# Kernel optimization log

Hardware: AMD Instinct MI355X
Metric: run time of the kernel (lower is better)

## Reference

```python
import jax, jax.numpy as jnp
import numpy as np

NUM_BINS = 8
TAIL = 3.0
MBW = 0.001  # min_bin_width
MBH = 0.001  # min_bin_height
MD = 0.001   # min_derivative


def _conv(x, w, b):
    y = jax.lax.conv_general_dilated(x, w, (1, 1), 'SAME',
                                     dimension_numbers=('NCHW', 'OIHW', 'NCHW'))
    return y + b[None, :, None, None]


def _convnet(x, w1, b1, w2, b2, w3, b3):
    h = jax.nn.relu(_conv(x, w1, b1))
    h = jax.nn.relu(_conv(h, w2, b2))
    return _conv(h, w3, b3)


def _rqs_forward(x, uw, uh, ud):
    # x: (N,), uw/uh: (N, num_bins), ud: (N, num_bins-1)
    nb = uw.shape[-1]
    inside = (x >= -TAIL) & (x <= TAIL)
    xin = jnp.clip(x, -TAIL, TAIL)
    # linear tails: pad derivatives so boundary slope == 1
    const = float(np.log(np.exp(1.0 - MD) - 1.0))
    ud = jnp.pad(ud, ((0, 0), (1, 1)), constant_values=const)

    widths = jax.nn.softmax(uw, axis=-1)
    widths = MBW + (1.0 - MBW * nb) * widths
    cumw = jnp.pad(jnp.cumsum(widths, axis=-1), ((0, 0), (1, 0)))
    cumw = 2.0 * TAIL * cumw - TAIL
    cumw = cumw.at[:, 0].set(-TAIL).at[:, -1].set(TAIL)
    widths = cumw[:, 1:] - cumw[:, :-1]

    heights = jax.nn.softmax(uh, axis=-1)
    heights = MBH + (1.0 - MBH * nb) * heights
    cumh = jnp.pad(jnp.cumsum(heights, axis=-1), ((0, 0), (1, 0)))
    cumh = 2.0 * TAIL * cumh - TAIL
    cumh = cumh.at[:, 0].set(-TAIL).at[:, -1].set(TAIL)
    heights = cumh[:, 1:] - cumh[:, :-1]

    deriv = MD + jax.nn.softplus(ud)  # (N, nb+1)

    # searchsorted: locate bin of each element
    idx = jnp.clip(jnp.sum((xin[:, None] >= cumw).astype(jnp.int32), axis=-1) - 1, 0, nb - 1)
    gather = lambda t: jnp.take_along_axis(t, idx[:, None], axis=-1)[:, 0]

    in_cw = gather(cumw)
    in_w = gather(widths)
    in_ch = gather(cumh)
    in_h = gather(heights)
    in_delta = gather(heights / widths)
    d0 = gather(deriv)
    d1 = gather(deriv[:, 1:])

    theta = (xin - in_cw) / in_w
    tom = theta * (1.0 - theta)
    numer = in_h * (in_delta * theta ** 2 + d0 * tom)
    denom = in_delta + (d0 + d1 - 2.0 * in_delta) * tom
    y = in_ch + numer / denom
    dnum = in_delta ** 2 * (d1 * theta ** 2 + 2.0 * in_delta * tom + d0 * (1.0 - theta) ** 2)
    lad = jnp.log(dnum) - 2.0 * jnp.log(denom)

    y = jnp.where(inside, y, x)
    lad = jnp.where(inside, lad, 0.0)
    return y, lad


def setup_inputs() -> dict:
    key = jax.random.key(0)
    ks = jax.random.split(key, 9)
    B, C, H, W = 32, 12, 64, 64
    hidden = 128
    cond_c = C // 3
    out_spline = C * (3 * NUM_BINS - 1)
    x = jax.random.normal(ks[0], (B, C, H, W), dtype=jnp.float32)
    logdet = jnp.zeros((B,), dtype=jnp.float32)
    conditioning = jax.random.normal(ks[1], (B, cond_c, H, W), dtype=jnp.float32)
    w1 = jax.random.normal(ks[2], (hidden, C + cond_c, 3, 3), dtype=jnp.float32) * 0.05
    b1 = jnp.zeros((hidden,), dtype=jnp.float32)
    w2 = jax.random.normal(ks[3], (hidden, hidden, 1, 1), dtype=jnp.float32) * 0.05
    b2 = jnp.zeros((hidden,), dtype=jnp.float32)
    w3 = jax.random.normal(ks[4], (out_spline, hidden, 3, 3), dtype=jnp.float32) * 0.01
    b3 = jnp.zeros((out_spline,), dtype=jnp.float32)
    return {"x": x, "logdet": logdet, "conditioning": conditioning,
            "w1": w1, "b1": b1, "w2": w2, "b2": b2, "w3": w3, "b3": b3}


def reference(x, logdet, conditioning, w1, b1, w2, b2, w3, b3):
    B, C, H, W = x.shape
    net_in = jnp.concatenate([x, conditioning], axis=1)
    params = _convnet(net_in, w1, b1, w2, b2, w3, b3)  # (B, C*(3nb-1), H, W)
    params = params.reshape(B, C, 3 * NUM_BINS - 1, H, W)
    params = params.transpose(0, 1, 3, 4, 2).reshape(B * C * H * W, 3 * NUM_BINS - 1)
    uw = params[:, :NUM_BINS]
    uh = params[:, NUM_BINS:2 * NUM_BINS]
    ud = params[:, 2 * NUM_BINS:]
    y_flat, lad_flat = _rqs_forward(x.reshape(-1), uw, uh, ud)
    y = y_flat.reshape(B, C, H, W)
    logdet_out = logdet + lad_flat.reshape(B, -1).sum(axis=1)
    return y, logdet_out
```

## Files before the change

### kernel.cpp

```cpp
#include <hip/hip_runtime.h>
#include <math.h>


#define NPIX 4096
#define NY   1572864

typedef _Float16 half8 __attribute__((ext_vector_type(8)));
typedef _Float16 half4 __attribute__((ext_vector_type(4)));
typedef float f32x4 __attribute__((ext_vector_type(4)));

#define ASYNC16(gsrc, ldst) \
  __builtin_amdgcn_global_load_lds((const __attribute__((address_space(1))) unsigned int*)(gsrc), \
                                   (__attribute__((address_space(3))) unsigned int*)(ldst), 16, 0, 0)

#define H2P_PLANE 4356
#define H2P_IDX(b, cc, pp) ((((size_t)(b) * 4 + (cc)) * H2P_PLANE + (pp)) << 5)
#define XH_IDX(b, pp) (((size_t)(b) * H2P_PLANE + (pp)) << 5)

__global__ __launch_bounds__(256) void prep_xh_k(
    const float* __restrict__ w1, const float* __restrict__ w2,
    const float* __restrict__ w3, _Float16* __restrict__ w1h,
    _Float16* __restrict__ w2h, _Float16* __restrict__ w3h,
    const float* __restrict__ logdet, float* __restrict__ ld_out,
    const float* __restrict__ x, const float* __restrict__ cond,
    _Float16* __restrict__ xh)
{
    const int i = blockIdx.x * 256 + threadIdx.x;
    if (i < 36864) {
        int k = i & 31, oc = (i >> 5) & 127, t = i >> 12;
        w1h[i] = (_Float16)((k < 16) ? w1[(oc * 16 + k) * 9 + t] : 0.f);
    }
    if (i < 16384) {
        int km = i & 31, oc = (i >> 5) & 127, ks = i >> 12;
        w2h[i] = (_Float16)w2[oc * 128 + ks * 32 + km];
    }
    {
        int cim = i & 31;
        int oc = (i >> 5) % 288;
        int tc = i / (288 * 32);
        int t = tc >> 2, cc = tc & 3;
        int c = oc / 24, j = oc % 24;
        int ci = cc * 32 + cim;
        float v = (j < 23) ? w3[((c * 23 + j) * 128 + ci) * 9 + t] : 0.f;
        w3h[i] = (_Float16)v;
    }
    if (i < 32) ld_out[i] = logdet[i];

    if (i < 139392) {
        const int b = i / H2P_PLANE, pp = i % H2P_PLANE;
        const int pr = pp / 66, pc = pp % 66;
        const bool interior = (pr >= 1) && (pr <= 64) && (pc >= 1) && (pc <= 64);
        _Float16 v[32];
#pragma unroll
        for (int ci = 0; ci < 32; ++ci) v[ci] = (_Float16)0.f;
        if (interior) {
            const int p = (pr - 1) * 64 + (pc - 1);
#pragma unroll
            for (int ci = 0; ci < 12; ++ci)
                v[ci] = (_Float16)x[((size_t)(b * 12 + ci) << 12) + p];
#pragma unroll
            for (int ci = 0; ci < 4; ++ci)
                v[12 + ci] = (_Float16)cond[((size_t)(b * 4 + ci) << 12) + p];
        }
        _Float16* dst = xh + ((size_t)i << 5);
#pragma unroll
        for (int q = 0; q < 4; ++q) *(f32x4*)(dst + q * 8) = *(f32x4*)(v + q * 8);
    }
}

__global__ __launch_bounds__(256, 2) void conv1_k(
    const _Float16* __restrict__ xh, const _Float16* __restrict__ w1h,
    const float* __restrict__ b1, _Float16* __restrict__ h1p)
{
    __shared__ __align__(16) char smem[73728];
    const int tid = threadIdx.x;
    const int wv = tid >> 6, lane = tid & 63;
    const int row16 = lane & 15, quad = lane >> 4;
    const int ptile = blockIdx.x;
    const int b = ptile >> 4;
    const int pim0 = (ptile & 15) << 8;
    const int h0 = pim0 >> 6;

#pragma unroll
    for (int k = 0; k < 18; ++k)
        ASYNC16(w1h + (size_t)(k * 256 + tid) * 8, smem + (k * 256 + wv * 64) * 16);

    f32x4 acc[4][8];
#pragma unroll
    for (int pt = 0; pt < 4; ++pt)
#pragma unroll
        for (int ot = 0; ot < 8; ++ot) acc[pt][ot] = (f32x4){0.f, 0.f, 0.f, 0.f};

    __syncthreads();
    const _Float16* wl = (const _Float16*)smem;

    for (int t = 0; t < 9; ++t) {
        const int dy = t / 3, dx = t % 3;
        const int pbase = (h0 + wv + dy) * 66 + dx + row16;
        half8 bf[4], af[8];
#pragma unroll
        for (int pt = 0; pt < 4; ++pt)
            bf[pt] = *(const half8*)(xh + XH_IDX(b, pbase + pt * 16) + quad * 8);
#pragma unroll
        for (int ot = 0; ot < 8; ++ot)
            af[ot] = *(const half8*)(wl + ((t * 128 + ot * 16 + row16) << 5) + quad * 8);
#pragma unroll
        for (int ot = 0; ot < 8; ++ot)
#pragma unroll
            for (int pt = 0; pt < 4; ++pt)
                acc[pt][ot] = __builtin_amdgcn_mfma_f32_16x16x32_f16(af[ot], bf[pt], acc[pt][ot], 0, 0, 0);
    }

    f32x4 bias[8];
#pragma unroll
    for (int ot = 0; ot < 8; ++ot) bias[ot] = *(const f32x4*)(b1 + ot * 16 + quad * 4);
#pragma unroll
    for (int pt = 0; pt < 4; ++pt) {
        const size_t pbase = ((size_t)((b << 12) + pim0 + wv * 64 + pt * 16 + row16)) << 7;
#pragma unroll
        for (int ot = 0; ot < 8; ++ot) {
            half4 v;
#pragma unroll
            for (int r = 0; r < 4; ++r)
                v[r] = (_Float16)fmaxf(acc[pt][ot][r] + bias[ot][r], 0.f);
            *(half4*)(h1p + pbase + ot * 16 + quad * 4) = v;
        }
    }
}

__global__ __launch_bounds__(256, 3) void conv2_k(
    const _Float16* __restrict__ h1p, const _Float16* __restrict__ w2h,
    const float* __restrict__ b2, _Float16* __restrict__ h2p)
{
    __shared__ __align__(16) char smem[33280];
    float* b2l = (float*)(smem + 32768);
    const int tid = threadIdx.x;
    const int wv = tid >> 6, lane = tid & 63;
    const int row16 = lane & 15, quad = lane >> 4;
    const int ptile = blockIdx.x;
    const int b = ptile >> 4;
    const int pim0 = (ptile & 15) << 8;

    if (tid < 128) b2l[tid] = b2[tid];
#pragma unroll
    for (int k = 0; k < 8; ++k) {
        const int c0 = k * 256 + wv * 64;
        ASYNC16(w2h + (size_t)(c0 + lane) * 8, smem + c0 * 16);
    }

    {
        const int base = blockIdx.x * 256 + tid;
#pragma unroll
        for (int rep = 0; rep < 2; ++rep) {
            const int i = base + rep * 131072;
            if (i < 133120) {
                const int q = i & 3;
                const int rest = i >> 2;
                const int r = rest % 260;
                const int cc2 = (rest / 260) & 3;
                const int bb = rest / 1040;
                int pp;
                if (r < 66)       pp = r;
                else if (r < 132) pp = 65 * 66 + (r - 66);
                else if (r < 196) pp = (r - 131) * 66;
                else              pp = (r - 195) * 66 + 65;
                f32x4 z = {0.f, 0.f, 0.f, 0.f};
                *(f32x4*)(h2p + H2P_IDX(bb, cc2, pp) + q * 8) = z;
            }
        }
    }

    f32x4 acc[4][8];
#pragma unroll
    for (int pt = 0; pt < 4; ++pt)
#pragma unroll
        for (int ot = 0; ot < 8; ++ot) acc[pt][ot] = (f32x4){0.f, 0.f, 0.f, 0.f};

    const int pixbase = (b << 12) + pim0 + wv * 64;
    __syncthreads();

#pragma unroll
    for (int ks = 0; ks < 4; ++ks) {
        half8 bf[4], af[8];
#pragma unroll
        for (int pt = 0; pt < 4; ++pt)
            bf[pt] = *(const half8*)(h1p + ((size_t)(pixbase + pt * 16 + row16) << 7) + ks * 32 + quad * 8);
        const _Float16* wl = (const _Float16*)smem;
#pragma unroll
        for (int ot = 0; ot < 8; ++ot)
            af[ot] = *(const half8*)(wl + ((ks * 128 + ot * 16 + row16) << 5) + quad * 8);
#pragma unroll
        for (int ot = 0; ot < 8; ++ot)
#pragma unroll
            for (int pt = 0; pt < 4; ++pt)
                acc[pt][ot] = __builtin_amdgcn_mfma_f32_16x16x32_f16(af[ot], bf[pt], acc[pt][ot], 0, 0, 0);
    }

#pragma unroll
    for (int pt = 0; pt < 4; ++pt) {
        const int p = pim0 + wv * 64 + pt * 16 + row16;
        const int pp = ((p >> 6) + 1) * 66 + (p & 63) + 1;
#pragma unroll
        for (int ot = 0; ot < 8; ++ot) {
            const int oc0 = ot * 16 + quad * 4;
            half4 v;
#pragma unroll
            for (int r = 0; r < 4; ++r)
                v[r] = (_Float16)fmaxf(acc[pt][ot][r] + b2l[oc0 + r], 0.f);
            *(half4*)(h2p + H2P_IDX(b, oc0 >> 5, pp) + (oc0 & 31)) = v;
        }
    }
}

__device__ __forceinline__ void rqs_eval(const f32x4* pv, float xv,
                                         float& yv_out, float& lad_out)
{
#define PRM(j) (pv[(j) >> 2][(j) & 3])
    const float xin = fminf(fmaxf(xv, -3.f), 3.f);

    float mw = PRM(0), mh = PRM(8);
#pragma unroll
    for (int j = 1; j < 8; ++j) { mw = fmaxf(mw, PRM(j)); mh = fmaxf(mh, PRM(8 + j)); }
    float ew[8], eh[8];
    float sw = 0.f, sh = 0.f;
#pragma unroll
    for (int j = 0; j < 8; ++j) {
        ew[j] = __expf(PRM(j) - mw);      sw += ew[j];
        eh[j] = __expf(PRM(8 + j) - mh);  sh += eh[j];
    }
    const float rw = 1.f / sw, rh = 1.f / sh;

    const float CONST_D = 0.5397423f;

    float cumw = 0.f, cumh = 0.f;
    float cw_lo = -3.f, ch_lo = -3.f;
    float in_cw = 0.f, in_w = 1.f, in_ch = 0.f, in_h = 1.f, sd0 = 0.f, sd1 = 0.f;
#pragma unroll
    for (int i = 0; i < 8; ++i) {
        cumw += fmaf(0.992f, ew[i] * rw, 0.001f);
        cumh += fmaf(0.992f, eh[i] * rh, 0.001f);
        const float cw_hi = (i == 7) ? 3.f : fmaf(6.f, cumw, -3.f);
        const float ch_hi = (i == 7) ? 3.f : fmaf(6.f, cumh, -3.f);
        const bool sel = (xin >= cw_lo) && ((i == 7) || (xin < cw_hi));
        in_cw = sel ? cw_lo : in_cw;
        in_w  = sel ? (cw_hi - cw_lo) : in_w;
        in_ch = sel ? ch_lo : in_ch;
        in_h  = sel ? (ch_hi - ch_lo) : in_h;
        sd0   = sel ? ((i == 0) ? CONST_D : PRM(16 + i - 1)) : sd0;
        sd1   = sel ? ((i == 7) ? CONST_D : PRM(16 + i)) : sd1;
        cw_lo = cw_hi; ch_lo = ch_hi;
    }

    const float d0 = 0.001f + ((sd0 > 20.f) ? sd0 : __logf(1.f + __expf(sd0)));
    const float d1 = 0.001f + ((sd1 > 20.f) ? sd1 : __logf(1.f + __expf(sd1)));

    const float r_inw = 1.f / in_w;
    const float delta = in_h * r_inw;
    const float theta = (xin - in_cw) * r_inw;
    const float omt = 1.f - theta;
    const float tom = theta * omt;
    const float th2 = theta * theta;
    const float numer = in_h * (delta * th2 + d0 * tom);
    const float denom = delta + (d0 + d1 - 2.f * delta) * tom;
    const float rden = 1.f / denom;
    float yv = in_ch + numer * rden;
    const float dnum = delta * delta * (d1 * th2 + 2.f * delta * tom + d0 * omt * omt);
    float lad = __logf(dnum * rden * rden);

    const bool inside = (xv >= -3.f) && (xv <= 3.f);
    yv_out = inside ? yv : xv;
    lad_out = inside ? lad : 0.f;
#undef PRM
}

__global__ __launch_bounds__(256, 2) void conv3_rqs_k(
    const _Float16* __restrict__ h2p, const _Float16* __restrict__ w3h,
    const float* __restrict__ b3, const float* __restrict__ x,
    float* __restrict__ y, float* __restrict__ ld_out)
{
    __shared__ __align__(16) char smem[62592];
    float* b3l = (float*)(smem + 62208);

    const int tid = threadIdx.x;
    const int wv = tid >> 6, lane = tid & 63;
    const int row16 = lane & 15, quad = lane >> 4;
    const int bid = blockIdx.x;
    const int g = bid / 24, r = bid % 24;
    const int col = r >> 3;
    const int ptile = (g << 3) | (r & 7);
    const int b = ptile >> 4;
    const int pim0 = (ptile & 15) << 8;
    const int h0 = pim0 >> 6;

    if (tid < 96) {
        const int c = tid / 24, j = tid % 24;
        b3l[tid] = (j < 23) ? b3[(col * 4 + c) * 23 + j] : 0.f;
    }

    f32x4 acc[4][6];
#pragma unroll
    for (int pt = 0; pt < 4; ++pt)
#pragma unroll
        for (int ot = 0; ot < 6; ++ot) acc[pt][ot] = (f32x4){0.f, 0.f, 0.f, 0.f};

    auto stage_wt3 = [&](int dy, int cc, int buf) {
#pragma unroll
        for (int j = 0; j < 3; ++j) {
            const int t = dy * 3 + j;
            const _Float16* gp = w3h + ((size_t)((t * 4 + cc) * 288 + col * 96) << 5);
            char* wb = smem + 25344 + buf * 18432 + j * 6144;
            ASYNC16(gp + (size_t)tid * 8, wb + wv * 1024);
            if (wv < 2) ASYNC16(gp + (size_t)(256 + tid) * 8, wb + 4096 + wv * 1024);
        }
    };
    auto stage_act = [&](int cc) {
        const _Float16* ga = h2p + H2P_IDX(b, cc, h0 * 66);
#pragma unroll
        for (int k = 0; k < 6; ++k)
            ASYNC16(ga + (size_t)(k * 256 + tid) * 8, smem + (k * 256 + wv * 64) * 16);
        if (wv == 0 && lane < 48)
            ASYNC16(ga + (size_t)(1536 + lane) * 8, smem + 1536 * 16);
    };

    stage_act(0);
    stage_wt3(0, 0, 0);

    for (int cc = 0; cc < 4; ++cc) {
        for (int dy = 0; dy < 3; ++dy) {
            const int step = cc * 3 + dy;
            __syncthreads();
            if (step + 1 < 12)
                stage_wt3((dy == 2) ? 0 : dy + 1, (dy == 2) ? cc + 1 : cc, (step + 1) & 1);
            const _Float16* act = (const _Float16*)smem;
            const _Float16* wt = (const _Float16*)(smem + 25344 + (step & 1) * 18432);
            const int lrow = (wv + dy) * 66 + row16;
#pragma unroll
            for (int dx = 0; dx < 3; ++dx) {
                half8 bf[4], af[6];
#pragma unroll
                for (int pt = 0; pt < 4; ++pt)
                    bf[pt] = *(const half8*)(act + ((lrow + dx + pt * 16) << 5) + quad * 8);
#pragma unroll
                for (int ot = 0; ot < 6; ++ot)
                    af[ot] = *(const half8*)(wt + dx * 3072 + ((ot * 16 + row16) << 5) + quad * 8);
#pragma unroll
                for (int ot = 0; ot < 6; ++ot)
#pragma unroll
                    for (int pt = 0; pt < 4; ++pt)
                        acc[pt][ot] = __builtin_amdgcn_mfma_f32_16x16x32_f16(af[ot], bf[pt], acc[pt][ot], 0, 0, 0);
            }
            if (dy == 2 && cc < 3) {
                __syncthreads();
                stage_act(cc + 1);
            }
        }
    }
    __syncthreads();

    float* epi = (float*)smem + wv * 1600;
    float lad_acc = 0.f;
#pragma unroll
    for (int pt = 0; pt < 4; ++pt) {
#pragma unroll
        for (int ot = 0; ot < 6; ++ot)
            *(f32x4*)(epi + row16 * 100 + ot * 16 + quad * 4) = acc[pt][ot];
        asm volatile("s_waitcnt lgkmcnt(0)" ::: "memory");
        __builtin_amdgcn_sched_barrier(0);
        {
            const int p16 = lane & 15, c = lane >> 4;
            const float* pb = epi + p16 * 100 + c * 24;
            const float* bb = b3l + c * 24;
            f32x4 pv[6];
#pragma unroll
            for (int q = 0; q < 6; ++q)
                pv[q] = *(const f32x4*)(pb + q * 4) + *(const f32x4*)(bb + q * 4);
            const int tpix = wv * 64 + pt * 16 + p16;
            const size_t xi = (((size_t)(b * 12 + col * 4 + c)) << 12) + (pim0 + tpix);
            const float xv = x[xi];
            float yv, lad;
            rqs_eval(pv, xv, yv, lad);
            y[xi] = yv;
            lad_acc += lad;
        }
        asm volatile("s_waitcnt lgkmcnt(0)" ::: "memory");
        __builtin_amdgcn_sched_barrier(0);
    }

#pragma unroll
    for (int off = 32; off > 0; off >>= 1) lad_acc += __shfl_down(lad_acc, off);
    if (lane == 0) atomicAdd(&ld_out[b], lad_acc);
}

extern "C" void kernel_launch(void* const* d_in, const int* in_sizes, int n_in,
                              void* d_out, int out_size, void* d_ws, size_t ws_size,
                              hipStream_t stream)
{
    const float* x      = (const float*)d_in[0];
    const float* logdet = (const float*)d_in[1];
    const float* cond   = (const float*)d_in[2];
    const float* w1     = (const float*)d_in[3];
    const float* b1     = (const float*)d_in[4];
    const float* w2     = (const float*)d_in[5];
    const float* b2     = (const float*)d_in[6];
    const float* w3     = (const float*)d_in[7];
    const float* b3     = (const float*)d_in[8];

    char* ws = (char*)d_ws;
    _Float16* h1p = (_Float16*)ws;
    _Float16* h2p = (_Float16*)(ws + 33554432);
    _Float16* xh  = (_Float16*)(ws + 33554432);
    _Float16* w1h = (_Float16*)(ws + 69238784);
    _Float16* w2h = (_Float16*)(ws + 69312512);
    _Float16* w3h = (_Float16*)(ws + 69345280);

    float* y      = (float*)d_out;
    float* ld_out = y + NY;

    prep_xh_k<<<1296, 256, 0, stream>>>(w1, w2, w3, w1h, w2h, w3h, logdet, ld_out, x, cond, xh);
    conv1_k<<<512, 256, 0, stream>>>(xh, w1h, b1, h1p);
    conv2_k<<<512, 256, 0, stream>>>(h1p, w2h, b2, h2p);
    conv3_rqs_k<<<1536, 256, 0, stream>>>(h2p, w3h, b3, x, y, ld_out);
}
```

Before: 223.0 us.

## Fuse conv1 and conv2 into one kernel keeping h1 tile in LDS

Merges the 3x3 conv1 and the 1x1 conv2 into a single kernel. The relu'd h1 tile is written to a padded LDS buffer instead of global memory, and conv2's weights are loaded into LDS alongside conv1's. This removes the global write and reread of h1 (32MB fp16) and one kernel launch. The h2p border zeroing moves into the prep kernel, and xh now lives at the start of the workspace since it no longer shares space with h2p. The cost is more LDS per block (~107KB), which drops occupancy to one block per CU.

```diff
diff --git a/kernel.cpp b/kernel.cpp
--- a/kernel.cpp
+++ b/kernel.cpp
@@ -2,7 +2,6 @@
 #include <math.h>
 
 
-#define NPIX 4096
 #define NY   1572864
 
 typedef _Float16 half8 __attribute__((ext_vector_type(8)));
@@ -23,7 +22,7 @@
     _Float16* __restrict__ w2h, _Float16* __restrict__ w3h,
     const float* __restrict__ logdet, float* __restrict__ ld_out,
     const float* __restrict__ x, const float* __restrict__ cond,
-    _Float16* __restrict__ xh)
+    _Float16* __restrict__ xh, _Float16* __restrict__ h2p)
 {
     const int i = blockIdx.x * 256 + threadIdx.x;
     if (i < 36864) {
@@ -46,6 +45,21 @@
     }
     if (i < 32) ld_out[i] = logdet[i];
 
+    if (i < 133120) {
+        const int q = i & 3;
+        const int rest = i >> 2;
+        const int r = rest % 260;
+        const int cc2 = (rest / 260) & 3;
+        const int bb = rest / 1040;
+        int pp;
+        if (r < 66)       pp = r;
+        else if (r < 132) pp = 65 * 66 + (r - 66);
+        else if (r < 196) pp = (r - 131) * 66;
+        else              pp = (r - 195) * 66 + 65;
+        f32x4 z = {0.f, 0.f, 0.f, 0.f};
+        *(f32x4*)(h2p + H2P_IDX(bb, cc2, pp) + q * 8) = z;
+    }
+
     if (i < 139392) {
         const int b = i / H2P_PLANE, pp = i % H2P_PLANE;
         const int pr = pp / 66, pc = pp % 66;
@@ -68,11 +82,15 @@
     }
 }
 
-__global__ __launch_bounds__(256, 2) void conv1_k(
+__global__ __launch_bounds__(256, 1) void conv12_k(
     const _Float16* __restrict__ xh, const _Float16* __restrict__ w1h,
-    const float* __restrict__ b1, _Float16* __restrict__ h1p)
-{
-    __shared__ __align__(16) char smem[73728];
+    const _Float16* __restrict__ w2h, const float* __restrict__ b1,
+    const float* __restrict__ b2, _Float16* __restrict__ h2p)
+{
+    __shared__ __align__(16) char smem[107008];
+    float* b2l = (float*)(smem + 106496);
+    _Float16* h1l = (_Float16*)smem;
+
     const int tid = threadIdx.x;
     const int wv = tid >> 6, lane = tid & 63;
     const int row16 = lane & 15, quad = lane >> 4;
@@ -81,9 +99,15 @@
     const int pim0 = (ptile & 15) << 8;
     const int h0 = pim0 >> 6;
 
+    if (tid < 128) b2l[tid] = b2[tid];
 #pragma unroll
     for (int k = 0; k < 18; ++k)
         ASYNC16(w1h + (size_t)(k * 256 + tid) * 8, smem + (k * 256 + wv * 64) * 16);
+#pragma unroll
+    for (int k = 0; k < 8; ++k) {
+        const int c0 = k * 256 + wv * 64;
+        ASYNC16(w2h + (size_t)(c0 + lane) * 8, smem + 73728 + c0 * 16);
+    }
 
     f32x4 acc[4][8];
 #pragma unroll
@@ -114,81 +138,35 @@
     f32x4 bias[8];
 #pragma unroll
     for (int ot = 0; ot < 8; ++ot) bias[ot] = *(const f32x4*)(b1 + ot * 16 + quad * 4);
+    __syncthreads();
 #pragma unroll
     for (int pt = 0; pt < 4; ++pt) {
-        const size_t pbase = ((size_t)((b << 12) + pim0 + wv * 64 + pt * 16 + row16)) << 7;
+        const int pix = wv * 64 + pt * 16 + row16;
 #pragma unroll
         for (int ot = 0; ot < 8; ++ot) {
             half4 v;
 #pragma unroll
             for (int r = 0; r < 4; ++r)
                 v[r] = (_Float16)fmaxf(acc[pt][ot][r] + bias[ot][r], 0.f);
-            *(half4*)(h1p + pbase + ot * 16 + quad * 4) = v;
-        }
-    }
-}
-
-__global__ __launch_bounds__(256, 3) void conv2_k(
-    const _Float16* __restrict__ h1p, const _Float16* __restrict__ w2h,
-    const float* __restrict__ b2, _Float16* __restrict__ h2p)
-{
-    __shared__ __align__(16) char smem[33280];
-    float* b2l = (float*)(smem + 32768);
-    const int tid = threadIdx.x;
-    const int wv = tid >> 6, lane = tid & 63;
-    const int row16 = lane & 15, quad = lane >> 4;
-    const int ptile = blockIdx.x;
-    const int b = ptile >> 4;
-    const int pim0 = (ptile & 15) << 8;
-
-    if (tid < 128) b2l[tid] = b2[tid];
-#pragma unroll
-    for (int k = 0; k < 8; ++k) {
-        const int c0 = k * 256 + wv * 64;
-        ASYNC16(w2h + (size_t)(c0 + lane) * 8, smem + c0 * 16);
-    }
-
-    {
-        const int base = blockIdx.x * 256 + tid;
-#pragma unroll
-        for (int rep = 0; rep < 2; ++rep) {
-            const int i = base + rep * 131072;
-            if (i < 133120) {
-                const int q = i & 3;
-                const int rest = i >> 2;
-                const int r = rest % 260;
-                const int cc2 = (rest / 260) & 3;
-                const int bb = rest / 1040;
-                int pp;
-                if (r < 66)       pp = r;
-                else if (r < 132) pp = 65 * 66 + (r - 66);
-                else if (r < 196) pp = (r - 131) * 66;
-                else              pp = (r - 195) * 66 + 65;
-                f32x4 z = {0.f, 0.f, 0.f, 0.f};
-                *(f32x4*)(h2p + H2P_IDX(bb, cc2, pp) + q * 8) = z;
-            }
-        }
-    }
-
-    f32x4 acc[4][8];
+            *(half4*)(h1l + pix * 136 + ot * 16 + quad * 4) = v;
+        }
+    }
 #pragma unroll
     for (int pt = 0; pt < 4; ++pt)
 #pragma unroll
         for (int ot = 0; ot < 8; ++ot) acc[pt][ot] = (f32x4){0.f, 0.f, 0.f, 0.f};
-
-    const int pixbase = (b << 12) + pim0 + wv * 64;
     __syncthreads();
 
+    const _Float16* w2l = (const _Float16*)(smem + 73728);
 #pragma unroll
     for (int ks = 0; ks < 4; ++ks) {
         half8 bf[4], af[8];
 #pragma unroll
         for (int pt = 0; pt < 4; ++pt)
-            bf[pt] = *(const half8*)(h1p + ((size_t)(pixbase + pt * 16 + row16) << 7) + ks * 32 + quad * 8);
-        const _Float16* wl = (const _Float16*)smem;
+            bf[pt] = *(const half8*)(h1l + (wv * 64 + pt * 16 + row16) * 136 + ks * 32 + quad * 8);
 #pragma unroll
         for (int ot = 0; ot < 8; ++ot)
-            af[ot] = *(const half8*)(wl + ((ks * 128 + ot * 16 + row16) << 5) + quad * 8);
+            af[ot] = *(const half8*)(w2l + ((ks * 128 + ot * 16 + row16) << 5) + quad * 8);
 #pragma unroll
         for (int ot = 0; ot < 8; ++ot)
 #pragma unroll
@@ -406,9 +384,8 @@
     const float* b3     = (const float*)d_in[8];
 
     char* ws = (char*)d_ws;
-    _Float16* h1p = (_Float16*)ws;
+    _Float16* xh  = (_Float16*)ws;
     _Float16* h2p = (_Float16*)(ws + 33554432);
-    _Float16* xh  = (_Float16*)(ws + 33554432);
     _Float16* w1h = (_Float16*)(ws + 69238784);
     _Float16* w2h = (_Float16*)(ws + 69312512);
     _Float16* w3h = (_Float16*)(ws + 69345280);
@@ -416,8 +393,7 @@
     float* y      = (float*)d_out;
     float* ld_out = y + NY;
 
-    prep_xh_k<<<1296, 256, 0, stream>>>(w1, w2, w3, w1h, w2h, w3h, logdet, ld_out, x, cond, xh);
-    conv1_k<<<512, 256, 0, stream>>>(xh, w1h, b1, h1p);
-    conv2_k<<<512, 256, 0, stream>>>(h1p, w2h, b2, h2p);
+    prep_xh_k<<<1296, 256, 0, stream>>>(w1, w2, w3, w1h, w2h, w3h, logdet, ld_out, x, cond, xh, h2p);
+    conv12_k<<<512, 256, 0, stream>>>(xh, w1h, w2h, b1, b2, h2p);
     conv3_rqs_k<<<1536, 256, 0, stream>>>(h2p, w3h, b3, x, y, ld_out);
 }
```

Measured after the change: 206.3 us. -7.5%, faster.
